# Kernel optimization log

Measured on AMD Instinct MI355X. Metric: run time of the kernel, lower is better.

The kernel has to match this reference:

```python
import jax, jax.numpy as jnp
import numpy as np

EPS = 1e-5


def _cbr(z, W, bn, relu=True):
    # z: [b, Cin, L]; W: [Cout, Cin]; bn: [4, Cout] = (gamma, beta, mean, var)
    # 1x1 Conv2d (bias=False) over a [b, Cin, L, 1] tensor == channel matmul.
    y = jnp.einsum('oi,bil->bol', W, z)
    g, b_, m, v = bn[0], bn[1], bn[2], bn[3]
    y = g[:, None] * (y - m[:, None]) * jax.lax.rsqrt(v[:, None] + EPS) + b_[:, None]
    return jax.nn.relu(y) if relu else y


def setup_inputs() -> dict:
    key = jax.random.key(0)
    ks = jax.random.split(key, 13)
    b, c, h, w = 32, 512, 48, 48
    in_spatial = h * w          # 2304
    inter_spatial = in_spatial // 4  # 576
    inter_channel = c // 4      # 128
    ncc = 1 + inter_channel     # 129
    return {
        'x': jax.random.normal(ks[0], (b, c, h, w), jnp.float32),
        'W_theta': jax.random.normal(ks[1], (inter_spatial, in_spatial), jnp.float32) * 0.02,
        'bn_theta': jax.random.uniform(ks[2], (4, inter_spatial), jnp.float32),
        'W_phi': jax.random.normal(ks[3], (inter_spatial, in_spatial), jnp.float32) * 0.02,
        'bn_phi': jax.random.uniform(ks[4], (4, inter_spatial), jnp.float32),
        'W_gx': jax.random.normal(ks[5], (inter_spatial, in_spatial), jnp.float32) * 0.02,
        'bn_gx': jax.random.uniform(ks[6], (4, inter_spatial), jnp.float32),
        'W_gg': jax.random.normal(ks[7], (inter_channel, 2 * c), jnp.float32) * 0.02,
        'bn_gg': jax.random.uniform(ks[8], (4, inter_channel), jnp.float32),
        'W_c1': jax.random.normal(ks[9], (ncc // 2, ncc), jnp.float32) * 0.02,
        'bn_c1': jax.random.uniform(ks[10], (4, ncc // 2), jnp.float32),
        'W_c2': jax.random.normal(ks[11], (1, ncc // 2), jnp.float32) * 0.02,
        'bn_c2': jax.random.uniform(ks[12], (4, 1), jnp.float32),
    }


def reference(x, W_theta, bn_theta, W_phi, bn_phi, W_gx, bn_gx,
              W_gg, bn_gg, W_c1, bn_c1, W_c2, bn_c2):
    b, c, h, w = x.shape
    xc = x.reshape(b, c, h * w).transpose(0, 2, 1)          # [b, hw, c]
    xc1 = _cbr(xc, W_theta, bn_theta).transpose(0, 2, 1)    # [b, c, is]
    xc2 = _cbr(xc, W_phi, bn_phi)                           # [b, is, c]
    Gc = jnp.einsum('bcs,bsd->bcd', xc1, xc2)               # [b, c, c]
    Gc_joint = jnp.concatenate([Gc.transpose(0, 2, 1), Gc], axis=1)  # [b, 2c, c]
    Gc_joint = _cbr(Gc_joint, W_gg, bn_gg)                  # [b, ic, c]
    g_xc = _cbr(xc, W_gx, bn_gx).mean(axis=1, keepdims=True)  # [b, 1, c]
    yc = jnp.concatenate([g_xc, Gc_joint], axis=1)          # [b, 1+ic, c]
    wy = _cbr(yc, W_c1, bn_c1)
    wy = _cbr(wy, W_c2, bn_c2, relu=False)                  # [b, 1, c]
    gate = jax.nn.sigmoid(wy)[:, 0, :, None, None]          # [b, c, 1, 1]
    return gate * x + x
```

## Files before the change

kernel.cpp:

```cpp
#include <hip/hip_runtime.h>
#include <cstdint>

#define EPSV 1e-5f
typedef unsigned short u16;
typedef __attribute__((ext_vector_type(8))) short bh8;
typedef __attribute__((ext_vector_type(4))) float f4;

__device__ __forceinline__ float bf2f(u16 h) { return __uint_as_float((unsigned)h << 16); }
__device__ __forceinline__ u16 f2bf(float x) {
    unsigned u = __float_as_uint(x);
    u += 0x7fffu + ((u >> 16) & 1u);
    return (u16)(u >> 16);
}

__device__ __forceinline__ void gl16(const void* g, const void* s) {
    __builtin_amdgcn_global_load_lds(
        reinterpret_cast<const __attribute__((address_space(1))) void*>((uintptr_t)g),
        reinterpret_cast<__attribute__((address_space(3))) void*>((unsigned)(uintptr_t)s),
        16, 0, 0);
}

__device__ __forceinline__ void stage_tiles(
    const u16* __restrict__ Ah, const u16* __restrict__ Al,
    const u16* __restrict__ Bh, const u16* __restrict__ Bl,
    size_t aoff, size_t boff, size_t ldA64, size_t ldB64,
    char* base, int s0)
{
    gl16(Ah + aoff + s0, base);
    gl16(Ah + aoff + ldA64 + s0, base + 4096);
    gl16(Al + aoff + s0, base + 8192);
    gl16(Al + aoff + ldA64 + s0, base + 12288);
    gl16(Bh + boff + s0, base + 16384);
    gl16(Bh + boff + ldB64 + s0, base + 20480);
    gl16(Bl + boff + s0, base + 24576);
    gl16(Bl + boff + ldB64 + s0, base + 28672);
}

__device__ __forceinline__ void core2(
    const u16* __restrict__ Ah, const u16* __restrict__ Al,
    const u16* __restrict__ Bh, const u16* __restrict__ Bl,
    long ldA, long ldB, int K, int rowA0, int rowB0,
    u16* lds, f4 acc[4][4])
{
    const int tid = threadIdx.x, l = tid & 63, w = tid >> 6;
    const int r0 = tid >> 2;
    const int c0e = (tid & 3) << 3;
    const int wr = w >> 1, wc = w & 1;
    const int lk = (l >> 4) << 3, lm = l & 15;
    const size_t aoff = (size_t)(rowA0 + r0) * ldA + c0e;
    const size_t boff = (size_t)(rowB0 + r0) * ldB + c0e;
    const size_t ldA64 = (size_t)64 * ldA, ldB64 = (size_t)64 * ldB;
    char* const base0 = (char*)lds + w * 1024;
    char* const base1 = (char*)lds + 32768 + w * 1024;
    const int nt = K >> 5;

    stage_tiles(Ah, Al, Bh, Bl, aoff, boff, ldA64, ldB64, base0, 0);
    __syncthreads();
    int p = 0;
    for (int t = 0; t < nt; ++t) {
        if (t + 1 < nt)
            stage_tiles(Ah, Al, Bh, Bl, aoff, boff, ldA64, ldB64,
                        p ? base0 : base1, (t + 1) << 5);
        const u16* buf = lds + p * 16384;
        bh8 a_h[4], a_l[4], b_h[4], b_l[4];
#pragma unroll
        for (int i = 0; i < 4; ++i) {
            const int ar = (wr * 64 + i * 16 + lm) * 32 + lk;
            const int br = (wc * 64 + i * 16 + lm) * 32 + lk;
            a_h[i] = *(const bh8*)&buf[ar];
            a_l[i] = *(const bh8*)&buf[4096 + ar];
            b_h[i] = *(const bh8*)&buf[8192 + br];
            b_l[i] = *(const bh8*)&buf[12288 + br];
        }
#pragma unroll
        for (int i = 0; i < 4; ++i)
#pragma unroll
            for (int j = 0; j < 4; ++j)
                acc[i][j] = __builtin_amdgcn_mfma_f32_16x16x32_bf16(a_h[i], b_h[j], acc[i][j], 0, 0, 0);
#pragma unroll
        for (int i = 0; i < 4; ++i)
#pragma unroll
            for (int j = 0; j < 4; ++j)
                acc[i][j] = __builtin_amdgcn_mfma_f32_16x16x32_bf16(a_h[i], b_l[j], acc[i][j], 0, 0, 0);
#pragma unroll
        for (int i = 0; i < 4; ++i)
#pragma unroll
            for (int j = 0; j < 4; ++j)
                acc[i][j] = __builtin_amdgcn_mfma_f32_16x16x32_bf16(a_l[i], b_h[j], acc[i][j], 0, 0, 0);
        __syncthreads();
        p ^= 1;
    }
}

__global__ __launch_bounds__(256) void gemm_s1_v3(
    const u16* __restrict__ Xh, const u16* __restrict__ Xl,
    const u16* __restrict__ W0h, const u16* __restrict__ W0l,
    const u16* __restrict__ W1h, const u16* __restrict__ W1l,
    const u16* __restrict__ W2h, const u16* __restrict__ W2l,
    const float* __restrict__ bn0, const float* __restrict__ bn1,
    const float* __restrict__ bn2,
    u16* __restrict__ Y0h, u16* __restrict__ Y0l,
    u16* __restrict__ Y1h, u16* __restrict__ Y1l,
    u16* __restrict__ Y2h, u16* __restrict__ Y2l)
{
    const int h = blockIdx.x;
    const int orig = (h & 7) * 240 + (h >> 3);
    const int ow = orig % 15;
    const int rest = orig / 15;
    const int ct = rest & 3, bz = rest >> 2;
    const int wi = ow / 5, otw = ow % 5;

    const u16* Bh = wi == 0 ? W0h : wi == 1 ? W1h : W2h;
    const u16* Bl = wi == 0 ? W0l : wi == 1 ? W1l : W2l;
    const float* bnp = wi == 0 ? bn0 : wi == 1 ? bn1 : bn2;
    u16* Yh = wi == 0 ? Y0h : wi == 1 ? Y1h : Y2h;
    u16* Yl = wi == 0 ? Y0l : wi == 1 ? Y1l : Y2l;

    __shared__ u16 lds[32768];
    f4 acc[4][4];
    const f4 z4 = {0.f, 0.f, 0.f, 0.f};
#pragma unroll
    for (int i = 0; i < 4; ++i)
#pragma unroll
        for (int j = 0; j < 4; ++j) acc[i][j] = z4;

    core2(Xh, Xl, Bh, Bl, 2304, 2304, 2304,
          bz * 512 + ct * 128, otw * 128, lds, acc);

    const int l = threadIdx.x & 63, w = threadIdx.x >> 6;
    const int wr = w >> 1, wc = w & 1;
    const int mb = ct * 128 + wr * 64;
    const int nbw = otw * 128 + wc * 64;
    const int lm = l & 15;
#pragma unroll
    for (int j = 0; j < 4; ++j) {
        const int o = nbw + j * 16 + lm;
        const bool val = (o < 576);
        float sc = 0.f, sh = 0.f;
        if (val) {
            const float gg = bnp[o], be = bnp[576 + o], mm = bnp[1152 + o], vv = bnp[1728 + o];
            sc = gg * rsqrtf(vv + EPSV);
            sh = be - mm * sc;
        }
#pragma unroll
        for (int i = 0; i < 4; ++i) {
            const int c = mb + i * 16 + ((l >> 4) << 2);
#pragma unroll
            for (int r = 0; r < 4; ++r) {
                const float y = val ? fmaxf(acc[i][j][r] * sc + sh, 0.f) : 0.f;
                const u16 hh = f2bf(y);
                const u16 lo = f2bf(y - bf2f(hh));
                const size_t off = ((size_t)bz * 512 + c + r) * 640 + o;
                Yh[off] = hh; Yl[off] = lo;
            }
        }
    }
}

__global__ __launch_bounds__(256) void gemm_u(
    const u16* __restrict__ Wggh, const u16* __restrict__ Wggl,
    const u16* __restrict__ tnth, const u16* __restrict__ tntl,
    const u16* __restrict__ pnth, const u16* __restrict__ pntl,
    u16* __restrict__ U1h, u16* __restrict__ U1l,
    u16* __restrict__ U2h, u16* __restrict__ U2l)
{
    const int h = blockIdx.x;
    const int orig = (h & 7) * 40 + (h >> 3);
    const int ot = orig % 5;
    const int rest = orig / 5;
    const int u = rest & 1, b = rest >> 1;

    const u16* Ah = Wggh + (u ? 512 : 0);
    const u16* Al = Wggl + (u ? 512 : 0);
    const u16* Bh = u ? tnth : pnth;
    const u16* Bl = u ? tntl : pntl;

    __shared__ u16 lds[32768];
    f4 acc[4][4];
    const f4 z4 = {0.f, 0.f, 0.f, 0.f};
#pragma unroll
    for (int i = 0; i < 4; ++i)
#pragma unroll
        for (int j = 0; j < 4; ++j) acc[i][j] = z4;

    core2(Ah, Al, Bh, Bl, 1024, 512, 512, 0, b * 640 + ot * 128, lds, acc);

    u16* Uh = u ? U2h : U1h;
    u16* Ul = u ? U2l : U1l;
    const int l = threadIdx.x & 63, w = threadIdx.x >> 6;
    const int wr = w >> 1, wc = w & 1;
#pragma unroll
    for (int i = 0; i < 4; ++i)
#pragma unroll
        for (int j = 0; j < 4; ++j)
#pragma unroll
            for (int r = 0; r < 4; ++r) {
                const int irow = wr * 64 + i * 16 + ((l >> 4) << 2) + r;
                const int ocol = ot * 128 + wc * 64 + j * 16 + (l & 15);
                const float v = acc[i][j][r];
                const u16 hh = f2bf(v);
                const u16 lo = f2bf(v - bf2f(hh));
                const size_t off = ((size_t)b * 128 + irow) * 640 + ocol;
                Uh[off] = hh; Ul[off] = lo;
            }
}

__global__ __launch_bounds__(256) void gemm_term(
    const u16* __restrict__ U1h, const u16* __restrict__ U1l,
    const u16* __restrict__ U2h, const u16* __restrict__ U2l,
    const u16* __restrict__ tth, const u16* __restrict__ ttl,
    const u16* __restrict__ pth, const u16* __restrict__ ptl,
    const float* __restrict__ bn, float* __restrict__ GG)
{
    const int h = blockIdx.x;
    const int orig = (h & 7) * 16 + (h >> 3);
    const int dt = orig & 3, b = orig >> 2;

    __shared__ u16 lds[32768];
    f4 acc[4][4];
    const f4 z4 = {0.f, 0.f, 0.f, 0.f};
#pragma unroll
    for (int i = 0; i < 4; ++i)
#pragma unroll
        for (int j = 0; j < 4; ++j) acc[i][j] = z4;

    core2(U1h, U1l, tth, ttl, 640, 640, 640,
          b * 128, b * 512 + dt * 128, lds, acc);
    core2(U2h, U2l, pth, ptl, 640, 640, 640,
          b * 128, b * 512 + dt * 128, lds, acc);

    const int l = threadIdx.x & 63, w = threadIdx.x >> 6;
    const int wr = w >> 1, wc = w & 1;
#pragma unroll
    for (int i = 0; i < 4; ++i)
#pragma unroll
        for (int r = 0; r < 4; ++r) {
            const int irow = wr * 64 + i * 16 + ((l >> 4) << 2) + r;
            const float g = bn[irow], be = bn[128 + irow], m = bn[256 + irow], v = bn[384 + irow];
            const float sc = g * rsqrtf(v + EPSV);
            const float sh = be - m * sc;
#pragma unroll
            for (int j = 0; j < 4; ++j) {
                const int dcol = dt * 128 + wc * 64 + j * 16 + (l & 15);
                GG[((size_t)b * 128 + irow) * 512 + dcol] =
                    fmaxf(acc[i][j][r] * sc + sh, 0.f);
            }
        }
}

__global__ __launch_bounds__(256) void transpose_y(
    const u16* __restrict__ s0, u16* __restrict__ d0,
    const u16* __restrict__ s1, u16* __restrict__ d1,
    const u16* __restrict__ s2, u16* __restrict__ d2,
    const u16* __restrict__ s3, u16* __restrict__ d3)
{
    const int pz = blockIdx.z;
    const int b = pz >> 2, pl = pz & 3;
    const u16* src = pl == 0 ? s0 : pl == 1 ? s1 : pl == 2 ? s2 : s3;
    u16* dst = pl == 0 ? d0 : pl == 1 ? d1 : pl == 2 ? d2 : d3;
    const int o0 = blockIdx.x * 64, c0 = blockIdx.y * 64;
    __shared__ u16 t[64][72];
    const int tid = threadIdx.x;
#pragma unroll
    for (int rdx = tid; rdx < 512; rdx += 256) {
        const int c = rdx >> 3, oc = (rdx & 7) << 3;
        *(bh8*)&t[c][oc] = *(const bh8*)&src[((size_t)b * 512 + c0 + c) * 640 + o0 + oc];
    }
    __syncthreads();
#pragma unroll
    for (int wdx = tid; wdx < 512; wdx += 256) {
        const int o = wdx >> 3, cc = (wdx & 7) << 3;
        u16 v[8];
#pragma unroll
        for (int e = 0; e < 8; ++e) v[e] = t[cc + e][o];
        *(bh8*)&dst[((size_t)b * 640 + o0 + o) * 512 + c0 + cc] = *(bh8*)&v[0];
    }
}

__global__ __launch_bounds__(256) void conv_split(
    const float* __restrict__ in, u16* __restrict__ hi, u16* __restrict__ lo, long n8)
{
    long i = (long)blockIdx.x * 256 + threadIdx.x;
    const long stride = (long)gridDim.x * 256;
    for (; i < n8; i += stride) {
        const float4 a = ((const float4*)in)[2 * i];
        const float4 b = ((const float4*)in)[2 * i + 1];
        const float v[8] = {a.x, a.y, a.z, a.w, b.x, b.y, b.z, b.w};
        unsigned hw[4], lw[4];
#pragma unroll
        for (int k = 0; k < 4; ++k) {
            const u16 h0 = f2bf(v[2 * k]), h1 = f2bf(v[2 * k + 1]);
            const u16 l0 = f2bf(v[2 * k] - bf2f(h0)), l1 = f2bf(v[2 * k + 1] - bf2f(h1));
            hw[k] = (unsigned)h0 | ((unsigned)h1 << 16);
            lw[k] = (unsigned)l0 | ((unsigned)l1 << 16);
        }
        *(uint4*)&hi[8 * i] = make_uint4(hw[0], hw[1], hw[2], hw[3]);
        *(uint4*)&lo[8 * i] = make_uint4(lw[0], lw[1], lw[2], lw[3]);
    }
}

__global__ __launch_bounds__(256) void conv_w_pad(
    const float* __restrict__ W, u16* __restrict__ hi, u16* __restrict__ lo,
    int rows, long n8)
{
    const long i = (long)blockIdx.x * 256 + threadIdx.x;
    if (i >= n8) return;
    const long e = i * 8;
    const int row = (int)(e / 2304);
    unsigned hw[4] = {0, 0, 0, 0}, lw[4] = {0, 0, 0, 0};
    if (row < rows) {
        const float4 a = ((const float4*)W)[2 * i];
        const float4 b = ((const float4*)W)[2 * i + 1];
        const float v[8] = {a.x, a.y, a.z, a.w, b.x, b.y, b.z, b.w};
#pragma unroll
        for (int k = 0; k < 4; ++k) {
            const u16 h0 = f2bf(v[2 * k]), h1 = f2bf(v[2 * k + 1]);
            const u16 l0 = f2bf(v[2 * k] - bf2f(h0)), l1 = f2bf(v[2 * k + 1] - bf2f(h1));
            hw[k] = (unsigned)h0 | ((unsigned)h1 << 16);
            lw[k] = (unsigned)l0 | ((unsigned)l1 << 16);
        }
    }
    *(uint4*)&hi[8 * i] = make_uint4(hw[0], hw[1], hw[2], hw[3]);
    *(uint4*)&lo[8 * i] = make_uint4(lw[0], lw[1], lw[2], lw[3]);
}

__global__ __launch_bounds__(256) void row_mean(
    const u16* __restrict__ Yh, const u16* __restrict__ Yl,
    float* __restrict__ out, int rows)
{
    const int l = threadIdx.x & 63;
    const int row = blockIdx.x * 4 + (threadIdx.x >> 6);
    if (row >= rows) return;
    const u16* ph = Yh + (size_t)row * 640;
    const u16* pl = Yl + (size_t)row * 640;
    float s = 0.f;
    struct U8 { u16 u[8]; };
    for (int k = l; k < 80; k += 64) {
        const U8 a = *(const U8*)&ph[k * 8];
        const U8 b = *(const U8*)&pl[k * 8];
#pragma unroll
        for (int e = 0; e < 8; ++e) s += bf2f(a.u[e]) + bf2f(b.u[e]);
    }
    for (int off = 32; off; off >>= 1) s += __shfl_down(s, off, 64);
    if (l == 0) out[row] = s * (1.f / 576.f);
}

__global__ __launch_bounds__(256)
void gate_kernel(const float* __restrict__ gxc, const float* __restrict__ GG,
                 const float* __restrict__ Wc1, const float* __restrict__ bn1,
                 const float* __restrict__ Wc2, const float* __restrict__ bn2,
                 float* __restrict__ gate, int IC, int D, int OC)
{
    const int b  = blockIdx.y;
    const int d0 = blockIdx.x * 64;

    __shared__ float yc_s[129][64];
    __shared__ float part[4][64];

    const int tid = threadIdx.x;
    for (int idx = tid; idx < 129 * 64; idx += 256) {
        const int j = idx >> 6, d = idx & 63;
        yc_s[j][d] = (j == 0) ? gxc[b * D + d0 + d]
                              : GG[((size_t)b * IC + (j - 1)) * D + d0 + d];
    }
    __syncthreads();

    const int d = tid & 63;
    const int q = tid >> 6;
    float acc2 = 0.f;
    for (int o = q * 16; o < q * 16 + 16; ++o) {
        float s = 0.f;
        const float* __restrict__ w = &Wc1[o * 129];
        for (int j = 0; j < 129; ++j) s = fmaf(w[j], yc_s[j][d], s);
        const float g1 = bn1[o], be1 = bn1[OC + o], m1 = bn1[2 * OC + o], v1 = bn1[3 * OC + o];
        const float sc = g1 / sqrtf(v1 + EPSV);
        const float w1 = fmaxf(s * sc + (be1 - m1 * sc), 0.f);
        acc2 = fmaf(Wc2[o], w1, acc2);
    }
    part[q][d] = acc2;
    __syncthreads();
    if (q == 0) {
        const float s = part[0][d] + part[1][d] + part[2][d] + part[3][d];
        const float g2 = bn2[0], be2 = bn2[1], m2 = bn2[2], v2 = bn2[3];
        const float sc = g2 / sqrtf(v2 + EPSV);
        const float wy = s * sc + (be2 - m2 * sc);
        gate[b * D + d0 + d] = 1.f / (1.f + expf(-wy));
    }
}

__global__ __launch_bounds__(256)
void final_kernel(const float* __restrict__ x, const float* __restrict__ gate,
                  float* __restrict__ out, long n4, int sp4)
{
    long i = (long)blockIdx.x * blockDim.x + threadIdx.x;
    const long stride = (long)gridDim.x * blockDim.x;
    for (; i < n4; i += stride) {
        float4 v = ((const float4*)x)[i];
        const long bc = i / sp4;
        const float gm = 1.f + gate[bc];
        v.x *= gm; v.y *= gm; v.z *= gm; v.w *= gm;
        ((float4*)out)[i] = v;
    }
}

extern "C" void kernel_launch(void* const* d_in, const int* in_sizes, int n_in,
                              void* d_out, int out_size, void* d_ws, size_t ws_size,
                              hipStream_t stream)
{
    const float* x        = (const float*)d_in[0];
    const float* W_theta  = (const float*)d_in[1];
    const float* bn_theta = (const float*)d_in[2];
    const float* W_phi    = (const float*)d_in[3];
    const float* bn_phi   = (const float*)d_in[4];
    const float* W_gx     = (const float*)d_in[5];
    const float* bn_gx    = (const float*)d_in[6];
    const float* W_gg     = (const float*)d_in[7];
    const float* bn_gg    = (const float*)d_in[8];
    const float* W_c1     = (const float*)d_in[9];
    const float* bn_c1    = (const float*)d_in[10];
    const float* W_c2     = (const float*)d_in[11];
    const float* bn_c2    = (const float*)d_in[12];
    float* out = (float*)d_out;

    const int B = 32, C = 512, S = 2304, O = 576, OP = 640, IC = 128, OC = 64;
    const size_t P  = (size_t)B * C * OP;
    const size_t WP = (size_t)OP * S;
    const size_t UP = (size_t)B * IC * OP;

    u16* tth = (u16*)d_out;
    u16* ttl = tth + P;
    u16* pth = ttl + P;
    u16* ptl = pth + P;
    u16* Wgh = ptl + P;
    u16* Wgl = Wgh + WP;
    u16* Wth = Wgl + WP;
    u16* Wtl = Wth + WP;
    u16* Wph = Wtl + WP;
    u16* Wpl = Wph + WP;
    u16* wggh = Wpl + WP;
    u16* wggl = wggh + (size_t)IC * 1024;
    u16* u1h = wggl + (size_t)IC * 1024;
    u16* u1l = u1h + UP;
    u16* u2h = u1l + UP;
    u16* u2l = u2h + UP;
    float* GG = (float*)(u2l + UP);

    u16* Xhi  = (u16*)d_ws;
    u16* Xlo  = Xhi + (size_t)B * C * S;
    u16* ygxh = Xlo + (size_t)B * C * S;
    u16* ygxl = ygxh + P;
    float* gxc  = (float*)(ygxl + P);
    float* gate = gxc + (size_t)B * C;
    u16* tnth = (u16*)d_ws;
    u16* tntl = tnth + P;
    u16* pnth = tntl + P;
    u16* pntl = pnth + P;

    const dim3 blk(256);

    const long wN8 = (long)WP / 8;
    conv_w_pad<<<dim3((unsigned)(wN8 / 256)), blk, 0, stream>>>(W_gx,    Wgh, Wgl, O, wN8);
    conv_w_pad<<<dim3((unsigned)(wN8 / 256)), blk, 0, stream>>>(W_theta, Wth, Wtl, O, wN8);
    conv_w_pad<<<dim3((unsigned)(wN8 / 256)), blk, 0, stream>>>(W_phi,   Wph, Wpl, O, wN8);
    conv_split<<<dim3(64), blk, 0, stream>>>(W_gg, wggh, wggl, (long)IC * 1024 / 8);

    conv_split<<<dim3(2048), blk, 0, stream>>>(x, Xhi, Xlo, (long)B * C * S / 8);
    gemm_s1_v3<<<dim3(1920), blk, 0, stream>>>(
        Xhi, Xlo, Wgh, Wgl, Wth, Wtl, Wph, Wpl,
        bn_gx, bn_theta, bn_phi,
        ygxh, ygxl, tth, ttl, pth, ptl);
    row_mean<<<dim3(4096), blk, 0, stream>>>(ygxh, ygxl, gxc, B * C);

    transpose_y<<<dim3(10, 8, 128), blk, 0, stream>>>(
        tth, tnth, ttl, tntl, pth, pnth, ptl, pntl);

    gemm_u<<<dim3(320), blk, 0, stream>>>(wggh, wggl, tnth, tntl, pnth, pntl,
                                          u1h, u1l, u2h, u2l);

    gemm_term<<<dim3(128), blk, 0, stream>>>(u1h, u1l, u2h, u2l,
                                             tth, ttl, pth, ptl, bn_gg, GG);

    gate_kernel<<<dim3(C / 64, B), blk, 0, stream>>>(gxc, GG, W_c1, bn_c1, W_c2, bn_c2,
                                                     gate, IC, C, OC);

    final_kernel<<<dim3(2048), blk, 0, stream>>>(x, gate, out,
                                                 (long)B * C * S / 4, S / 4);
}
```

Before: 695.5 us.

## Split gemm_term K-reduction across blocks and switch LDS staging to fragment-major layout

gemm_term's two chained K-loops (U1·theta and U2·phi) are split into separate blocks, doubling the grid from 128 to 256 workgroups. Partial sums go to two fp32 buffers, and a new gg_combine kernel adds them and applies BN plus ReLU. Separately, the shared core2 staging now writes global_load_lds tiles in the MFMA fragment order, so each lane reads its fragment with one contiguous 16-byte LDS load, aiming to remove bank conflicts. The cost is an extra launch plus extra fp32 traffic for writing and re-reading the partial buffers.

```diff
diff --git a/kernel.cpp b/kernel.cpp
--- a/kernel.cpp
+++ b/kernel.cpp
@@ -20,22 +20,6 @@
         16, 0, 0);
 }
 
-__device__ __forceinline__ void stage_tiles(
-    const u16* __restrict__ Ah, const u16* __restrict__ Al,
-    const u16* __restrict__ Bh, const u16* __restrict__ Bl,
-    size_t aoff, size_t boff, size_t ldA64, size_t ldB64,
-    char* base, int s0)
-{
-    gl16(Ah + aoff + s0, base);
-    gl16(Ah + aoff + ldA64 + s0, base + 4096);
-    gl16(Al + aoff + s0, base + 8192);
-    gl16(Al + aoff + ldA64 + s0, base + 12288);
-    gl16(Bh + boff + s0, base + 16384);
-    gl16(Bh + boff + ldB64 + s0, base + 20480);
-    gl16(Bl + boff + s0, base + 24576);
-    gl16(Bl + boff + ldB64 + s0, base + 28672);
-}
-
 __device__ __forceinline__ void core2(
     const u16* __restrict__ Ah, const u16* __restrict__ Al,
     const u16* __restrict__ Bh, const u16* __restrict__ Bl,
@@ -43,34 +27,39 @@
     u16* lds, f4 acc[4][4])
 {
     const int tid = threadIdx.x, l = tid & 63, w = tid >> 6;
-    const int r0 = tid >> 2;
-    const int c0e = (tid & 3) << 3;
     const int wr = w >> 1, wc = w & 1;
-    const int lk = (l >> 4) << 3, lm = l & 15;
-    const size_t aoff = (size_t)(rowA0 + r0) * ldA + c0e;
-    const size_t boff = (size_t)(rowB0 + r0) * ldB + c0e;
-    const size_t ldA64 = (size_t)64 * ldA, ldB64 = (size_t)64 * ldB;
-    char* const base0 = (char*)lds + w * 1024;
-    char* const base1 = (char*)lds + 32768 + w * 1024;
+    const int lm = l & 15, lq = l >> 4;
+    const size_t aoff = (size_t)(rowA0 + lm) * ldA + lq * 8;
+    const size_t boff = (size_t)(rowB0 + lm) * ldB + lq * 8;
+    const size_t a16 = (size_t)16 * ldA, b16 = (size_t)16 * ldB;
+    char* const base0 = (char*)lds;
+    char* const base1 = (char*)lds + 32768;
     const int nt = K >> 5;
 
-    stage_tiles(Ah, Al, Bh, Bl, aoff, boff, ldA64, ldB64, base0, 0);
+#define STAGE_FM(base, s0) do { \
+    gl16(Ah + aoff + (size_t)(w)     * a16 + (s0), (base) +         w * 1024); \
+    gl16(Ah + aoff + (size_t)(w + 4) * a16 + (s0), (base) +  4096 + w * 1024); \
+    gl16(Al + aoff + (size_t)(w)     * a16 + (s0), (base) +  8192 + w * 1024); \
+    gl16(Al + aoff + (size_t)(w + 4) * a16 + (s0), (base) + 12288 + w * 1024); \
+    gl16(Bh + boff + (size_t)(w)     * b16 + (s0), (base) + 16384 + w * 1024); \
+    gl16(Bh + boff + (size_t)(w + 4) * b16 + (s0), (base) + 20480 + w * 1024); \
+    gl16(Bl + boff + (size_t)(w)     * b16 + (s0), (base) + 24576 + w * 1024); \
+    gl16(Bl + boff + (size_t)(w + 4) * b16 + (s0), (base) + 28672 + w * 1024); \
+} while (0)
+
+    STAGE_FM(base0, 0);
     __syncthreads();
     int p = 0;
     for (int t = 0; t < nt; ++t) {
-        if (t + 1 < nt)
-            stage_tiles(Ah, Al, Bh, Bl, aoff, boff, ldA64, ldB64,
-                        p ? base0 : base1, (t + 1) << 5);
-        const u16* buf = lds + p * 16384;
+        if (t + 1 < nt) STAGE_FM(p ? base0 : base1, (size_t)(t + 1) << 5);
+        const char* buf = p ? base1 : base0;
         bh8 a_h[4], a_l[4], b_h[4], b_l[4];
 #pragma unroll
         for (int i = 0; i < 4; ++i) {
-            const int ar = (wr * 64 + i * 16 + lm) * 32 + lk;
-            const int br = (wc * 64 + i * 16 + lm) * 32 + lk;
-            a_h[i] = *(const bh8*)&buf[ar];
-            a_l[i] = *(const bh8*)&buf[4096 + ar];
-            b_h[i] = *(const bh8*)&buf[8192 + br];
-            b_l[i] = *(const bh8*)&buf[12288 + br];
+            a_h[i] = *(const bh8*)(buf + (wr * 4 + i) * 1024 + l * 16);
+            a_l[i] = *(const bh8*)(buf + 8192 + (wr * 4 + i) * 1024 + l * 16);
+            b_h[i] = *(const bh8*)(buf + 16384 + (wc * 4 + i) * 1024 + l * 16);
+            b_l[i] = *(const bh8*)(buf + 24576 + (wc * 4 + i) * 1024 + l * 16);
         }
 #pragma unroll
         for (int i = 0; i < 4; ++i)
@@ -90,6 +79,7 @@
         __syncthreads();
         p ^= 1;
     }
+#undef STAGE_FM
 }
 
 __global__ __launch_bounds__(256) void gemm_s1_v3(
@@ -205,16 +195,24 @@
             }
 }
 
-__global__ __launch_bounds__(256) void gemm_term(
+__global__ __launch_bounds__(256) void gemm_term_p(
     const u16* __restrict__ U1h, const u16* __restrict__ U1l,
     const u16* __restrict__ U2h, const u16* __restrict__ U2l,
     const u16* __restrict__ tth, const u16* __restrict__ ttl,
     const u16* __restrict__ pth, const u16* __restrict__ ptl,
-    const float* __restrict__ bn, float* __restrict__ GG)
+    float* __restrict__ GGa, float* __restrict__ GGb)
 {
     const int h = blockIdx.x;
-    const int orig = (h & 7) * 16 + (h >> 3);
-    const int dt = orig & 3, b = orig >> 2;
+    const int orig = (h & 7) * 32 + (h >> 3);
+    const int dt = orig & 3;
+    const int u = (orig >> 2) & 1;
+    const int b = orig >> 3;
+
+    const u16* Ah = u ? U2h : U1h;
+    const u16* Al = u ? U2l : U1l;
+    const u16* Bh = u ? pth : tth;
+    const u16* Bl = u ? ptl : ttl;
+    float* G = u ? GGb : GGa;
 
     __shared__ u16 lds[32768];
     f4 acc[4][4];
@@ -224,9 +222,7 @@
 #pragma unroll
         for (int j = 0; j < 4; ++j) acc[i][j] = z4;
 
-    core2(U1h, U1l, tth, ttl, 640, 640, 640,
-          b * 128, b * 512 + dt * 128, lds, acc);
-    core2(U2h, U2l, pth, ptl, 640, 640, 640,
+    core2(Ah, Al, Bh, Bl, 640, 640, 640,
           b * 128, b * 512 + dt * 128, lds, acc);
 
     const int l = threadIdx.x & 63, w = threadIdx.x >> 6;
@@ -234,18 +230,32 @@
 #pragma unroll
     for (int i = 0; i < 4; ++i)
 #pragma unroll
-        for (int r = 0; r < 4; ++r) {
-            const int irow = wr * 64 + i * 16 + ((l >> 4) << 2) + r;
-            const float g = bn[irow], be = bn[128 + irow], m = bn[256 + irow], v = bn[384 + irow];
-            const float sc = g * rsqrtf(v + EPSV);
-            const float sh = be - m * sc;
-#pragma unroll
-            for (int j = 0; j < 4; ++j) {
+        for (int j = 0; j < 4; ++j)
+#pragma unroll
+            for (int r = 0; r < 4; ++r) {
+                const int irow = wr * 64 + i * 16 + ((l >> 4) << 2) + r;
                 const int dcol = dt * 128 + wc * 64 + j * 16 + (l & 15);
-                GG[((size_t)b * 128 + irow) * 512 + dcol] =
-                    fmaxf(acc[i][j][r] * sc + sh, 0.f);
+                G[((size_t)b * 128 + irow) * 512 + dcol] = acc[i][j][r];
             }
-        }
+}
+
+__global__ __launch_bounds__(256) void gg_combine(
+    float* __restrict__ GGa, const float* __restrict__ GGb,
+    const float* __restrict__ bn, long n4)
+{
+    const long i = (long)blockIdx.x * 256 + threadIdx.x;
+    if (i >= n4) return;
+    const int irow = (int)((i >> 7) & 127);
+    const float g = bn[irow], be = bn[128 + irow], m = bn[256 + irow], v = bn[384 + irow];
+    const float sc = g * rsqrtf(v + EPSV);
+    const float sh = be - m * sc;
+    float4 a = ((const float4*)GGa)[i];
+    const float4 b = ((const float4*)GGb)[i];
+    a.x = fmaxf((a.x + b.x) * sc + sh, 0.f);
+    a.y = fmaxf((a.y + b.y) * sc + sh, 0.f);
+    a.z = fmaxf((a.z + b.z) * sc + sh, 0.f);
+    a.w = fmaxf((a.w + b.w) * sc + sh, 0.f);
+    ((float4*)GGa)[i] = a;
 }
 
 __global__ __launch_bounds__(256) void transpose_y(
@@ -443,7 +453,8 @@
     u16* u1l = u1h + UP;
     u16* u2h = u1l + UP;
     u16* u2l = u2h + UP;
-    float* GG = (float*)(u2l + UP);
+    float* GGa = (float*)(u2l + UP);
+    float* GGb = GGa + (size_t)B * IC * C;
 
     u16* Xhi  = (u16*)d_ws;
     u16* Xlo  = Xhi + (size_t)B * C * S;
@@ -477,10 +488,12 @@
     gemm_u<<<dim3(320), blk, 0, stream>>>(wggh, wggl, tnth, tntl, pnth, pntl,
                                           u1h, u1l, u2h, u2l);
 
-    gemm_term<<<dim3(128), blk, 0, stream>>>(u1h, u1l, u2h, u2l,
-                                             tth, ttl, pth, ptl, bn_gg, GG);
-
-    gate_kernel<<<dim3(C / 64, B), blk, 0, stream>>>(gxc, GG, W_c1, bn_c1, W_c2, bn_c2,
+    gemm_term_p<<<dim3(256), blk, 0, stream>>>(u1h, u1l, u2h, u2l,
+                                               tth, ttl, pth, ptl, GGa, GGb);
+    gg_combine<<<dim3(2048), blk, 0, stream>>>(GGa, GGb, bn_gg,
+                                               (long)B * IC * C / 4);
+
+    gate_kernel<<<dim3(C / 64, B), blk, 0, stream>>>(gxc, GGa, W_c1, bn_c1, W_c2, bn_c2,
                                                      gate, IC, C, OC);
 
     final_kernel<<<dim3(2048), blk, 0, stream>>>(x, gate, out,
```

Result: slower. 856.4 us (+23.1%).
